# Kernel tuning notes

Measured on AMD Instinct MI355X. Metric: run time of the kernel, lower is better.

The kernel has to match this reference:

```python
import jax, jax.numpy as jnp
import numpy as np

TEMP = 0.07  # module hardcodes self.temp = 0.07 regardless of ctor arg
N, C = 8192, 256


def setup_inputs() -> dict:
    key = jax.random.key(0)
    kq, kk = jax.random.split(key)
    q = jax.random.normal(kq, (N, C), dtype=jnp.float32)
    k = jax.random.normal(kk, (N, C), dtype=jnp.float32)
    return {"q": q, "k": k}


def reference(q, k):
    # Original builds logits = [l_pos, l_neg_row] per sample i where
    # l_pos = q_i . k_i and l_neg_row = q_i . k_j for j != i, then applies
    # CrossEntropyLoss with label 0. That logits row is exactly a permutation
    # of the full similarity row sim[i, :] = q_i @ k.T (diagonal = positive),
    # so CE(logits/T, 0) == logsumexp(sim_i/T) - sim_ii/T. Single fused GEMM
    # + row-wise logsumexp, identical math and gradients.
    sim = jnp.matmul(q, k.T) / TEMP            # [N, N]
    pos = jnp.diagonal(sim)                    # [N]
    lse = jax.nn.logsumexp(sim, axis=1)        # [N]
    return jnp.mean(lse - pos)                 # scalar loss
```

## Files before the change

kernel.cpp:

```cpp
#include <hip/hip_runtime.h>
#include <stdint.h>


#define N_ROWS 8192
#define C_DIM  256
#define BN     32
#define SPLIT  16
#define JCOLS  (N_ROWS / SPLIT)
#define JTILES (JCOLS / BN)
#define BLK_ROWS 128
#define TILE_B  (BN * C_DIM * 2)

typedef __attribute__((ext_vector_type(8)))  _Float16 half8;
typedef __attribute__((ext_vector_type(4)))  _Float16 half4;
typedef __attribute__((ext_vector_type(16))) float    f32x16;

#if __has_builtin(__builtin_amdgcn_exp2f)
#define EXP2(x) __builtin_amdgcn_exp2f(x)
#else
#define EXP2(x) exp2f(x)
#endif
#if __has_builtin(__builtin_amdgcn_logf)
#define LOG2(x) __builtin_amdgcn_logf(x)
#else
#define LOG2(x) log2f(x)
#endif

__device__ __forceinline__ void gload_lds16(const void* g, void* l) {
  __builtin_amdgcn_global_load_lds(
      (const __attribute__((address_space(1))) unsigned int*)g,
      (__attribute__((address_space(3))) unsigned int*)l, 16, 0, 0);
}

__global__ void cvt_kernel(const float* __restrict__ q, const float* __restrict__ k,
                           _Float16* __restrict__ qh, _Float16* __restrict__ kh,
                           float* __restrict__ pP) {
  const float QS = 20.60992915555663f;
  int i = blockIdx.x * 256 + threadIdx.x;
  float4 qv = ((const float4*)q)[i];
  float4 kv = ((const float4*)k)[i];
  half4 qo, ko;
  qo[0] = (_Float16)(qv.x * QS); qo[1] = (_Float16)(qv.y * QS);
  qo[2] = (_Float16)(qv.z * QS); qo[3] = (_Float16)(qv.w * QS);
  ko[0] = (_Float16)kv.x; ko[1] = (_Float16)kv.y;
  ko[2] = (_Float16)kv.z; ko[3] = (_Float16)kv.w;
  ((half4*)qh)[i] = qo;
  ((half4*)kh)[i] = ko;

  float d = (float)qo[0] * (float)ko[0];
  d = fmaf((float)qo[1], (float)ko[1], d);
  d = fmaf((float)qo[2], (float)ko[2], d);
  d = fmaf((float)qo[3], (float)ko[3], d);
#pragma unroll
  for (int off = 1; off < 64; off <<= 1) d += __shfl_xor(d, off);
  if ((threadIdx.x & 63) == 0) pP[i >> 6] = d;
}

__launch_bounds__(256, 3)
__global__ void sim_lse_kernel(const _Float16* __restrict__ qh,
                               const _Float16* __restrict__ kh,
                               float* __restrict__ pM,
                               float* __restrict__ pS) {
  __shared__ __align__(16) _Float16 kt[2 * BN * C_DIM];
  const int tid  = threadIdx.x;
  const int lane = tid & 63;
  const int wave = tid >> 6;
  const int r    = lane & 31;
  const int hi   = lane >> 5;

  const int bid  = blockIdx.x;
  const int sp   = bid & (SPLIT - 1);
  const int rb   = bid >> 4;
  const int row0 = rb * BLK_ROWS + wave * 32;

  half8 a[16];
  {
    const _Float16* qr = qh + (size_t)(row0 + r) * C_DIM + hi * 8;
#pragma unroll
    for (int ks = 0; ks < 16; ++ks) a[ks] = *(const half8*)(qr + ks * 16);
  }

  float M[16], S[16];
#pragma unroll
  for (int j = 0; j < 16; ++j) { M[j] = -__builtin_inff(); S[j] = 0.f; }

  const int bb = r * 512 + ((hi ^ r) << 4);

  const char* ksrc = (const char*)(kh + (size_t)sp * JCOLS * C_DIM);
  char* lds = (char*)kt;

#pragma unroll
  for (int it = 0; it < 4; ++it) {
    int linear = it * 4096 + tid * 16;
    int row = linear >> 9;
    int gc  = ((linear >> 4) & 31) ^ row;
    gload_lds16(ksrc + row * 512 + gc * 16, lds + linear);
  }

  for (int jt = 0; jt < JTILES; ++jt) {
    __syncthreads();
    const char* cur = lds + (jt & 1) * TILE_B;

    if (jt + 1 < JTILES) {
      const char* src = ksrc + (size_t)(jt + 1) * TILE_B;
      char* nxt = lds + ((jt + 1) & 1) * TILE_B;
#pragma unroll
      for (int it = 0; it < 4; ++it) {
        int linear = it * 4096 + tid * 16;
        int row = linear >> 9;
        int gc  = ((linear >> 4) & 31) ^ row;
        gload_lds16(src + row * 512 + gc * 16, nxt + linear);
      }
    }

    f32x16 acc;
#pragma unroll
    for (int j = 0; j < 16; ++j) acc[j] = 0.f;

#pragma unroll
    for (int ks = 0; ks < 16; ++ks) {
      half8 b = *(const half8*)(cur + (bb ^ (ks * 32)));
      acc = __builtin_amdgcn_mfma_f32_32x32x16_f16(a[ks], b, acc, 0, 0, 0);
    }

#pragma unroll
    for (int j = 0; j < 16; ++j) {
      float v = acc[j];
      float newM  = fmaxf(M[j], v);
      float alpha = EXP2(M[j] - newM);
      float p     = EXP2(v - newM);
      S[j] = fmaf(S[j], alpha, p);
      M[j] = newM;
    }
  }

#pragma unroll
  for (int j = 0; j < 16; ++j) {
#pragma unroll
    for (int off = 1; off < 32; off <<= 1) {
      float Mo = __shfl_xor(M[j], off);
      float So = __shfl_xor(S[j], off);
      float nm = fmaxf(M[j], Mo);
      S[j] = S[j] * EXP2(M[j] - nm) + So * EXP2(Mo - nm);
      M[j] = nm;
    }
  }

  if ((lane & 31) == 0) {
#pragma unroll
    for (int j = 0; j < 16; ++j) {
      int grow = row0 + (j & 3) + 8 * (j >> 2) + 4 * hi;
      pM[(size_t)sp * N_ROWS + grow] = M[j];
      pS[(size_t)sp * N_ROWS + grow] = S[j];
    }
  }
}

__global__ void finish1_kernel(const float* __restrict__ pM, const float* __restrict__ pS,
                               const float* __restrict__ pP, float* __restrict__ pPart) {
  const int tid = threadIdx.x;
  const int r = blockIdx.x * 256 + tid;
  float m = -__builtin_inff();
#pragma unroll
  for (int s = 0; s < SPLIT; ++s) m = fmaxf(m, pM[s * N_ROWS + r]);
  float ssum = 0.f;
#pragma unroll
  for (int s = 0; s < SPLIT; ++s)
    ssum = fmaf(pS[s * N_ROWS + r], EXP2(pM[s * N_ROWS + r] - m), ssum);
  float accl = (m + LOG2(ssum)) - pP[r];
#pragma unroll
  for (int off = 1; off < 64; off <<= 1) accl += __shfl_xor(accl, off);
  __shared__ float wsum[4];
  if ((tid & 63) == 0) wsum[tid >> 6] = accl;
  __syncthreads();
  if (tid == 0)
    pPart[blockIdx.x] = wsum[0] + wsum[1] + wsum[2] + wsum[3];
}

__global__ void finish2_kernel(const float* __restrict__ pPart, float* __restrict__ out) {
  const int tid = threadIdx.x;
  float v = (tid < 32) ? pPart[tid] : 0.f;
#pragma unroll
  for (int off = 1; off < 64; off <<= 1) v += __shfl_xor(v, off);
  if (tid == 0)
    out[0] = v * (0.69314718055994531f / (float)N_ROWS);
}

extern "C" void kernel_launch(void* const* d_in, const int* in_sizes, int n_in,
                              void* d_out, int out_size, void* d_ws, size_t ws_size,
                              hipStream_t stream) {
  const float* q = (const float*)d_in[0];
  const float* k = (const float*)d_in[1];
  float* out = (float*)d_out;
  char* ws = (char*)d_ws;

  _Float16* qh = (_Float16*)ws;
  _Float16* kh = (_Float16*)(ws + (size_t)N_ROWS * C_DIM * 2);
  float* pM = (float*)(ws + (size_t)N_ROWS * C_DIM * 4);
  float* pS = pM + SPLIT * N_ROWS;
  float* pP = pS + SPLIT * N_ROWS;
  float* pPart = pP + N_ROWS;

  cvt_kernel<<<dim3(N_ROWS * C_DIM / 4 / 256), dim3(256), 0, stream>>>(q, k, qh, kh, pP);
  sim_lse_kernel<<<dim3((N_ROWS / BLK_ROWS) * SPLIT), dim3(256), 0, stream>>>(qh, kh, pM, pS);
  finish1_kernel<<<dim3(N_ROWS / 256), dim3(256), 0, stream>>>(pM, pS, pP, pPart);
  finish2_kernel<<<dim3(1), dim3(64), 0, stream>>>(pPart, out);
}
```

Measured before the change: 125.5 us.

## Switch sim GEMM to 16x16x32 MFMA with 2x2 fragment tiling

Replaces the single 32x32x16 MFMA per K-step with four 16x16x32 MFMAs covering a 2x2 grid of 16x16 fragments per wave, and restructures A registers, LDS swizzled B reads, online-softmax state and reductions to match. Each accumulator element now merges two columns per exp update, halving the rescale (alpha) exps per logit, and the final cross-lane reduction spans 16 lanes instead of 32. Occupancy hint is lowered from 3 to 2 blocks per SIMD, which allows more registers but may reduce latency hiding.

```diff
diff --git a/kernel.cpp b/kernel.cpp
--- a/kernel.cpp
+++ b/kernel.cpp
@@ -13,7 +13,7 @@
 
 typedef __attribute__((ext_vector_type(8)))  _Float16 half8;
 typedef __attribute__((ext_vector_type(4)))  _Float16 half4;
-typedef __attribute__((ext_vector_type(16))) float    f32x16;
+typedef __attribute__((ext_vector_type(4)))  float    f32x4;
 
 #if __has_builtin(__builtin_amdgcn_exp2f)
 #define EXP2(x) __builtin_amdgcn_exp2f(x)
@@ -56,7 +56,7 @@
   if ((threadIdx.x & 63) == 0) pP[i >> 6] = d;
 }
 
-__launch_bounds__(256, 3)
+__launch_bounds__(256, 2)
 __global__ void sim_lse_kernel(const _Float16* __restrict__ qh,
                                const _Float16* __restrict__ kh,
                                float* __restrict__ pM,
@@ -65,26 +65,30 @@
   const int tid  = threadIdx.x;
   const int lane = tid & 63;
   const int wave = tid >> 6;
-  const int r    = lane & 31;
-  const int hi   = lane >> 5;
+  const int l15  = lane & 15;
+  const int lg   = lane >> 4;
 
   const int bid  = blockIdx.x;
   const int sp   = bid & (SPLIT - 1);
   const int rb   = bid >> 4;
   const int row0 = rb * BLK_ROWS + wave * 32;
 
-  half8 a[16];
-  {
-    const _Float16* qr = qh + (size_t)(row0 + r) * C_DIM + hi * 8;
-#pragma unroll
-    for (int ks = 0; ks < 16; ++ks) a[ks] = *(const half8*)(qr + ks * 16);
-  }
-
-  float M[16], S[16];
-#pragma unroll
-  for (int j = 0; j < 16; ++j) { M[j] = -__builtin_inff(); S[j] = 0.f; }
-
-  const int bb = r * 512 + ((hi ^ r) << 4);
+  half8 a[2][8];
+#pragma unroll
+  for (int rf = 0; rf < 2; ++rf) {
+    const _Float16* qr = qh + (size_t)(row0 + rf * 16 + l15) * C_DIM + lg * 8;
+#pragma unroll
+    for (int ks = 0; ks < 8; ++ks) a[rf][ks] = *(const half8*)(qr + ks * 32);
+  }
+
+  float M[8], S[8];
+#pragma unroll
+  for (int s = 0; s < 8; ++s) { M[s] = -__builtin_inff(); S[s] = 0.f; }
+
+  const int nl0 = l15;
+  const int nl1 = 16 + l15;
+  const int bb0 = nl0 * 512 + (((nl0 & 31) * 16) ^ (lg * 16));
+  const int bb1 = nl1 * 512 + (((nl1 & 31) * 16) ^ (lg * 16));
 
   const char* ksrc = (const char*)(kh + (size_t)sp * JCOLS * C_DIM);
   char* lds = (char*)kt;
@@ -93,7 +97,7 @@
   for (int it = 0; it < 4; ++it) {
     int linear = it * 4096 + tid * 16;
     int row = linear >> 9;
-    int gc  = ((linear >> 4) & 31) ^ row;
+    int gc  = ((linear >> 4) & 31) ^ (row & 31);
     gload_lds16(ksrc + row * 512 + gc * 16, lds + linear);
   }
 
@@ -108,50 +112,63 @@
       for (int it = 0; it < 4; ++it) {
         int linear = it * 4096 + tid * 16;
         int row = linear >> 9;
-        int gc  = ((linear >> 4) & 31) ^ row;
+        int gc  = ((linear >> 4) & 31) ^ (row & 31);
         gload_lds16(src + row * 512 + gc * 16, nxt + linear);
       }
     }
 
-    f32x16 acc;
-#pragma unroll
-    for (int j = 0; j < 16; ++j) acc[j] = 0.f;
-
-#pragma unroll
-    for (int ks = 0; ks < 16; ++ks) {
-      half8 b = *(const half8*)(cur + (bb ^ (ks * 32)));
-      acc = __builtin_amdgcn_mfma_f32_32x32x16_f16(a[ks], b, acc, 0, 0, 0);
-    }
-
-#pragma unroll
-    for (int j = 0; j < 16; ++j) {
-      float v = acc[j];
-      float newM  = fmaxf(M[j], v);
-      float alpha = EXP2(M[j] - newM);
-      float p     = EXP2(v - newM);
-      S[j] = fmaf(S[j], alpha, p);
-      M[j] = newM;
-    }
-  }
-
-#pragma unroll
-  for (int j = 0; j < 16; ++j) {
-#pragma unroll
-    for (int off = 1; off < 32; off <<= 1) {
-      float Mo = __shfl_xor(M[j], off);
-      float So = __shfl_xor(S[j], off);
-      float nm = fmaxf(M[j], Mo);
-      S[j] = S[j] * EXP2(M[j] - nm) + So * EXP2(Mo - nm);
-      M[j] = nm;
-    }
-  }
-
-  if ((lane & 31) == 0) {
-#pragma unroll
-    for (int j = 0; j < 16; ++j) {
-      int grow = row0 + (j & 3) + 8 * (j >> 2) + 4 * hi;
-      pM[(size_t)sp * N_ROWS + grow] = M[j];
-      pS[(size_t)sp * N_ROWS + grow] = S[j];
+    f32x4 acc00 = {0.f,0.f,0.f,0.f}, acc01 = {0.f,0.f,0.f,0.f};
+    f32x4 acc10 = {0.f,0.f,0.f,0.f}, acc11 = {0.f,0.f,0.f,0.f};
+
+#pragma unroll
+    for (int ks = 0; ks < 8; ++ks) {
+      half8 b0 = *(const half8*)(cur + (bb0 ^ (ks * 64)));
+      half8 b1 = *(const half8*)(cur + (bb1 ^ (ks * 64)));
+      acc00 = __builtin_amdgcn_mfma_f32_16x16x32_f16(a[0][ks], b0, acc00, 0, 0, 0);
+      acc01 = __builtin_amdgcn_mfma_f32_16x16x32_f16(a[0][ks], b1, acc01, 0, 0, 0);
+      acc10 = __builtin_amdgcn_mfma_f32_16x16x32_f16(a[1][ks], b0, acc10, 0, 0, 0);
+      acc11 = __builtin_amdgcn_mfma_f32_16x16x32_f16(a[1][ks], b1, acc11, 0, 0, 0);
+    }
+
+#pragma unroll
+    for (int j = 0; j < 4; ++j) {
+      {
+        float v0 = acc00[j], v1 = acc01[j];
+        float newM  = fmaxf(M[j], fmaxf(v0, v1));
+        float alpha = EXP2(M[j] - newM);
+        float p = EXP2(v0 - newM) + EXP2(v1 - newM);
+        S[j] = fmaf(S[j], alpha, p);
+        M[j] = newM;
+      }
+      {
+        float v0 = acc10[j], v1 = acc11[j];
+        float newM  = fmaxf(M[4 + j], fmaxf(v0, v1));
+        float alpha = EXP2(M[4 + j] - newM);
+        float p = EXP2(v0 - newM) + EXP2(v1 - newM);
+        S[4 + j] = fmaf(S[4 + j], alpha, p);
+        M[4 + j] = newM;
+      }
+    }
+  }
+
+#pragma unroll
+  for (int s = 0; s < 8; ++s) {
+#pragma unroll
+    for (int off = 1; off < 16; off <<= 1) {
+      float Mo = __shfl_xor(M[s], off);
+      float So = __shfl_xor(S[s], off);
+      float nm = fmaxf(M[s], Mo);
+      S[s] = S[s] * EXP2(M[s] - nm) + So * EXP2(Mo - nm);
+      M[s] = nm;
+    }
+  }
+
+  if (l15 == 0) {
+#pragma unroll
+    for (int s = 0; s < 8; ++s) {
+      int grow = row0 + (s >> 2) * 16 + lg * 4 + (s & 3);
+      pM[(size_t)sp * N_ROWS + grow] = M[s];
+      pS[(size_t)sp * N_ROWS + grow] = S[s];
     }
   }
 }
```

New measurement: 112.6 us. 10.2% less time.
